# Performance work log

Measured on AMD Instinct MI355X. Metric: run time of the kernel, lower is better.

The kernel has to match this reference:

```python
import jax, jax.numpy as jnp
import numpy as np

T, N, D, H = 128, 512, 1024, 1024
LN_EPS = 1e-5


def setup_inputs() -> dict:
    key = jax.random.key(0)
    ks = jax.random.split(key, 6)
    x = jax.random.normal(ks[0], (T * N, D), jnp.float32)
    hxs = jax.random.normal(ks[1], (N, 1, H), jnp.float32)
    # binary done-masks (float, mostly 1.0 = keep hidden state, 0.0 = episode reset)
    masks = (jax.random.uniform(ks[2], (T * N, 1)) < 0.95).astype(jnp.float32)
    s = 1.0 / np.sqrt(H)
    # PyTorch GRU packed gates, order (r, z, n): weight_ih_l0 [3H, D], weight_hh_l0 [3H, H]
    W_ih = jax.random.normal(ks[3], (3 * H, D), jnp.float32) * s
    W_hh = jax.random.normal(ks[4], (3 * H, H), jnp.float32) * s
    b_ih = jnp.zeros((3 * H,), jnp.float32)  # module inits biases to 0
    b_hh = jnp.zeros((3 * H,), jnp.float32)
    gamma = jnp.ones((H,), jnp.float32)
    beta = jnp.zeros((H,), jnp.float32)
    return dict(x=x, hxs=hxs, masks=masks, W_ih=W_ih, W_hh=W_hh,
                b_ih=b_ih, b_hh=b_hh, gamma=gamma, beta=beta)


def reference(x, hxs, masks, W_ih, W_hh, b_ih, b_hh, gamma, beta):
    TN = x.shape[0]
    Nn = hxs.shape[0]
    Tt = TN // Nn
    Hd = hxs.shape[-1]
    xs = x.reshape(Tt, Nn, -1)          # [T, N, D]
    m = masks.reshape(Tt, Nn)           # [T, N]
    # Chunk starts per source: t=0 plus every t>=1 where (masks[t] == 1).any().
    # At a chunk start the hidden state is multiplied by masks[t] (broadcast over layers);
    # a scan with a per-step conditional mask-multiply is exactly equivalent to the
    # torch loop over chunks.
    reset = jnp.concatenate([jnp.ones((1,), bool), jnp.any(m[1:] == 1.0, axis=-1)])
    # Batch the input projection across all T*N tokens (one big GEMM): [T, N, 3H]
    xp = jnp.einsum('tnd,gd->tng', xs, W_ih) + b_ih
    h0 = hxs[:, 0, :]                   # recurrent_N == 1 -> [N, H]

    def step(h, inp):
        xp_t, m_t, r_t = inp
        h = jnp.where(r_t, h * m_t[:, None], h)
        hp = h @ W_hh.T + b_hh          # [N, 3H]
        xr, xz, xn = jnp.split(xp_t, 3, axis=-1)
        hr, hz, hn = jnp.split(hp, 3, axis=-1)
        r = jax.nn.sigmoid(xr + hr)
        z = jax.nn.sigmoid(xz + hz)
        n = jnp.tanh(xn + r * hn)
        h_new = (1.0 - z) * n + z * h
        return h_new, h_new

    h_last, outs = jax.lax.scan(step, h0, (xp, m, reset))
    y = outs.reshape(Tt * Nn, Hd)
    # LayerNorm over last dim
    mu = y.mean(-1, keepdims=True)
    var = y.var(-1, keepdims=True)
    y = (y - mu) * jax.lax.rsqrt(var + LN_EPS) * gamma + beta
    return y, h_last[:, None, :]
```

## Files before the change

kernel.cpp:

```cpp
#include <hip/hip_runtime.h>

#define T_STEPS 128
#define N_B     512
#define D_IN    1024
#define H_DIM   1024
#define G_DIM   3072
#define M_ALL   (T_STEPS * N_B)

typedef short          s8v  __attribute__((ext_vector_type(8)));
typedef float          f4v  __attribute__((ext_vector_type(4)));
typedef unsigned short u4v  __attribute__((ext_vector_type(4)));

__device__ __forceinline__ unsigned short f2bf(float f) {
  union { float f; unsigned u; } v; v.f = f;
  unsigned r = v.u + 0x7FFFu + ((v.u >> 16) & 1u);
  return (unsigned short)(r >> 16);
}
__device__ __forceinline__ float bf2f(unsigned short h) {
  union { unsigned u; float f; } v; v.u = ((unsigned)h) << 16;
  return v.f;
}
__device__ __forceinline__ void async16(const void* g, void* l) {
  __builtin_amdgcn_global_load_lds(
      (const __attribute__((address_space(1))) unsigned*)g,
      (__attribute__((address_space(3))) unsigned*)l, 16, 0, 0);
}
__device__ __forceinline__ float sigmoidf_(float x) { return 1.f / (1.f + __expf(-x)); }
__device__ __forceinline__ float tanhf_(float x)    { return 1.f - 2.f / (1.f + __expf(2.f * x)); }

__global__ void cvt_bf16(const float* __restrict__ in, unsigned short* __restrict__ out, long n4) {
  long i = (long)blockIdx.x * blockDim.x + threadIdx.x;
  long stride = (long)gridDim.x * blockDim.x;
  for (; i < n4; i += stride) {
    f4v v = *(const f4v*)(in + i * 4);
    u4v o;
    #pragma unroll
    for (int e = 0; e < 4; ++e) o[e] = f2bf(v[e]);
    *(u4v*)(out + i * 4) = o;
  }
}

__global__ void reset_kernel(const float* __restrict__ masks, int* __restrict__ reset) {
  const int t = blockIdx.x;
  __shared__ int flag;
  if (threadIdx.x == 0) flag = (t == 0) ? 1 : 0;
  __syncthreads();
  if (t > 0 && masks[(size_t)t * N_B + threadIdx.x] == 1.0f) flag = 1;
  __syncthreads();
  if (threadIdx.x == 0) reset[t] = flag;
}

__global__ __launch_bounds__(256) void gemm_xp(const unsigned short* __restrict__ A,
                                               const unsigned short* __restrict__ B,
                                               const float* __restrict__ bias,
                                               unsigned short* __restrict__ C) {
  const int m0 = blockIdx.y * 128, g0 = blockIdx.x * 128;
  const int tid = threadIdx.x, wv = tid >> 6, l = tid & 63;
  const int l15 = l & 15, l4 = l >> 4;
  const int wr = wv >> 1, wc = wv & 1;
  __shared__ unsigned short As[128 * 64], Bs[128 * 64];

  f4v zero4 = {0.f, 0.f, 0.f, 0.f};
  f4v acc[4][4];
  #pragma unroll
  for (int i = 0; i < 4; ++i)
    #pragma unroll
    for (int j = 0; j < 4; ++j) acc[i][j] = zero4;

  const int srow = l >> 3;
  const int selem = (l & 7) * 8;

  for (int kt = 0; kt < 1024; kt += 64) {
    #pragma unroll
    for (int cc = 0; cc < 4; ++cc) {
      int s = wv * 4 + cc;
      int row = s * 8 + srow;
      async16(A + (size_t)(m0 + row) * 1024 + kt + selem, &As[s * 512]);
      async16(B + (size_t)(g0 + row) * 1024 + kt + selem, &Bs[s * 512]);
    }
    __syncthreads();
    #pragma unroll
    for (int ks = 0; ks < 2; ++ks) {
      s8v a[4], b[4];
      #pragma unroll
      for (int i = 0; i < 4; ++i) {
        a[i] = *(const s8v*)&As[(wr * 64 + i * 16 + l15) * 64 + ks * 32 + l4 * 8];
        b[i] = *(const s8v*)&Bs[(wc * 64 + i * 16 + l15) * 64 + ks * 32 + l4 * 8];
      }
      #pragma unroll
      for (int i = 0; i < 4; ++i)
        #pragma unroll
        for (int j = 0; j < 4; ++j)
          acc[i][j] = __builtin_amdgcn_mfma_f32_16x16x32_bf16(a[i], b[j], acc[i][j], 0, 0, 0);
    }
    __syncthreads();
  }
  #pragma unroll
  for (int j = 0; j < 4; ++j) {
    int gcol = g0 + wc * 64 + j * 16 + l15;
    float bv = bias[gcol];
    #pragma unroll
    for (int i = 0; i < 4; ++i) {
      int mrow = m0 + wr * 64 + i * 16 + l4 * 4;
      #pragma unroll
      for (int r = 0; r < 4; ++r)
        C[(size_t)(mrow + r) * G_DIM + gcol] = f2bf(acc[i][j][r] + bv);
    }
  }
}

__global__ __launch_bounds__(256) void gru_step6(
    const unsigned short* __restrict__ Whh,
    const unsigned short* __restrict__ xp,
    const float* __restrict__ masks,
    const int* __restrict__ reset,
    const float* __restrict__ bhh,
    const float* __restrict__ hxs,
    const unsigned short* __restrict__ hread,
    unsigned short* __restrict__ hwrite,
    float* __restrict__ y,
    float* __restrict__ hlast,
    int t) {
  const int bid = blockIdx.x;
  const int jt = bid & 31, nt = bid >> 5;
  const int j0 = jt * 32, n0 = nt * 64;
  const int tid = threadIdx.x, w = tid >> 6, l = tid & 63;
  const int l15 = l & 15, l4 = l >> 4;
  const int wn = w & 1, wj = w >> 1;
  const size_t NH = (size_t)N_B * H_DIM;

  __shared__ unsigned short Hs[3][64 * 128];
  __shared__ unsigned short Ws[3][96 * 128];

  const int lrow4 = l >> 4;
  const int lcb = (l & 15) * 16;
  const int swz_rd = (l15 & 7) << 4;

  const int jj = j0 + wj * 16 + l15;
  const int rst = reset[t];
  const unsigned short* xpt = xp + (size_t)t * N_B * G_DIM;

  bool zo[2];
  #pragma unroll
  for (int i = 0; i < 2; ++i) {
    float mv = masks[(size_t)t * N_B + n0 + wn * 32 + i * 16 + l15];
    zo[i] = rst && (mv == 0.0f);
  }
  const float* hsrc = (t == 0) ? hxs : (y + (size_t)(t - 1) * NH);
  float hreg[2][4], mreg[2][4];
  unsigned short xpr[2][4][3];
  #pragma unroll
  for (int i = 0; i < 2; ++i)
    #pragma unroll
    for (int r = 0; r < 4; ++r) {
      const int n = n0 + wn * 32 + i * 16 + l4 * 4 + r;
      hreg[i][r] = hsrc[(size_t)n * H_DIM + jj];
      mreg[i][r] = masks[(size_t)t * N_B + n];
      const size_t xo = (size_t)n * G_DIM + jj;
      #pragma unroll
      for (int g3 = 0; g3 < 3; ++g3)
        xpr[i][r][g3] = xpt[xo + (size_t)g3 * H_DIM];
    }
  const float br = bhh[jj];
  const float bz = bhh[H_DIM + jj];
  const float bn = bhh[2 * H_DIM + jj];

  f4v zero4 = {0.f, 0.f, 0.f, 0.f};
  s8v zer8 = {0, 0, 0, 0, 0, 0, 0, 0};
  f4v acc[2][3];
  #pragma unroll
  for (int i = 0; i < 2; ++i)
    #pragma unroll
    for (int g3 = 0; g3 < 3; ++g3) acc[i][g3] = zero4;

  auto stage = [&](int buf, int kt) {
    #pragma unroll
    for (int q = 0; q < 4; ++q) {
      int rb = w * 16 + q * 4;
      int row = rb + lrow4;
      int cb = lcb ^ ((row & 7) << 4);
      async16(hread + (size_t)(n0 + row) * H_DIM + kt * 128 + (cb >> 1), &Hs[buf][rb * 128]);
    }
    #pragma unroll
    for (int q = 0; q < 6; ++q) {
      int rb = w * 24 + q * 4;
      int row = rb + lrow4;
      int gate = row >> 5, jjl = row & 31;
      int cb = lcb ^ ((row & 7) << 4);
      async16(Whh + ((size_t)gate * H_DIM + j0 + jjl) * H_DIM + kt * 128 + (cb >> 1),
              &Ws[buf][rb * 128]);
    }
  };

  stage(0, 0);
  stage(1, 1);

  #pragma unroll
  for (int kt = 0; kt < 8; ++kt) {
    if (kt < 7) asm volatile("s_waitcnt vmcnt(10)" ::: "memory");
    else        asm volatile("s_waitcnt vmcnt(0)"  ::: "memory");
    __builtin_amdgcn_s_barrier();
    __builtin_amdgcn_sched_barrier(0);
    if (kt < 6) stage((kt + 2) % 3, kt + 2);
    const char* hb = (const char*)&Hs[kt % 3][0];
    const char* wb = (const char*)&Ws[kt % 3][0];
    #pragma unroll
    for (int ks = 0; ks < 4; ++ks) {
      const int kbb = (ks * 64 + l4 * 16) ^ swz_rd;
      s8v a[2], b[3];
      #pragma unroll
      for (int i = 0; i < 2; ++i) {
        a[i] = *(const s8v*)(hb + (wn * 32 + i * 16 + l15) * 256 + kbb);
        if (zo[i]) a[i] = zer8;
      }
      #pragma unroll
      for (int g3 = 0; g3 < 3; ++g3)
        b[g3] = *(const s8v*)(wb + (g3 * 32 + wj * 16 + l15) * 256 + kbb);
      #pragma unroll
      for (int i = 0; i < 2; ++i)
        #pragma unroll
        for (int g3 = 0; g3 < 3; ++g3)
          acc[i][g3] = __builtin_amdgcn_mfma_f32_16x16x32_bf16(a[i], b[g3], acc[i][g3], 0, 0, 0);
    }
  }

  #pragma unroll
  for (int i = 0; i < 2; ++i) {
    #pragma unroll
    for (int r = 0; r < 4; ++r) {
      const int n = n0 + wn * 32 + i * 16 + l4 * 4 + r;
      float hprev = hreg[i][r];
      if (rst && mreg[i][r] == 0.0f) hprev = 0.0f;
      const float hr = acc[i][0][r] + br;
      const float hz = acc[i][1][r] + bz;
      const float hn = acc[i][2][r] + bn;
      const float xr = bf2f(xpr[i][r][0]);
      const float xz = bf2f(xpr[i][r][1]);
      const float xn = bf2f(xpr[i][r][2]);
      const float rg = sigmoidf_(xr + hr);
      const float zg = sigmoidf_(xz + hz);
      const float ng = tanhf_(xn + rg * hn);
      const float hnew = (1.f - zg) * ng + zg * hprev;
      const size_t gidx = (size_t)n * H_DIM + jj;
      y[(size_t)t * NH + gidx] = hnew;
      hwrite[gidx] = f2bf(hnew);
      if (t == T_STEPS - 1) hlast[gidx] = hnew;
    }
  }
}

__global__ __launch_bounds__(256) void ln_kernel(float* __restrict__ y,
                                                 const float* __restrict__ gamma,
                                                 const float* __restrict__ beta) {
  const size_t row = blockIdx.x;
  float* p = y + row * (size_t)H_DIM;
  const int tid = threadIdx.x;
  f4v v = *(const f4v*)(p + tid * 4);
  float s = v[0] + v[1] + v[2] + v[3];
  float q = v[0] * v[0] + v[1] * v[1] + v[2] * v[2] + v[3] * v[3];
  #pragma unroll
  for (int off = 32; off > 0; off >>= 1) {
    s += __shfl_down(s, off);
    q += __shfl_down(q, off);
  }
  __shared__ float sb[8];
  const int wid = tid >> 6, lid = tid & 63;
  if (lid == 0) { sb[wid] = s; sb[4 + wid] = q; }
  __syncthreads();
  float S = sb[0] + sb[1] + sb[2] + sb[3];
  float Q = sb[4] + sb[5] + sb[6] + sb[7];
  float mean = S * (1.f / H_DIM);
  float var = Q * (1.f / H_DIM) - mean * mean;
  float inv = rsqrtf(var + 1e-5f);
  f4v g4 = *(const f4v*)(gamma + tid * 4);
  f4v b4 = *(const f4v*)(beta + tid * 4);
  f4v o;
  #pragma unroll
  for (int e = 0; e < 4; ++e) o[e] = (v[e] - mean) * inv * g4[e] + b4[e];
  *(f4v*)(p + tid * 4) = o;
}

extern "C" void kernel_launch(void* const* d_in, const int* in_sizes, int n_in,
                              void* d_out, int out_size, void* d_ws, size_t ws_size,
                              hipStream_t stream) {
  const float* x     = (const float*)d_in[0];
  const float* hxs   = (const float*)d_in[1];
  const float* masks = (const float*)d_in[2];
  const float* W_ih  = (const float*)d_in[3];
  const float* W_hh  = (const float*)d_in[4];
  const float* b_ih  = (const float*)d_in[5];
  const float* b_hh  = (const float*)d_in[6];
  const float* gamma = (const float*)d_in[7];
  const float* beta  = (const float*)d_in[8];
  float* y = (float*)d_out;
  float* hlast = y + (size_t)T_STEPS * N_B * H_DIM;

  char* ws = (char*)d_ws;
  unsigned short* Wih_bf = (unsigned short*)ws;  ws += (size_t)G_DIM * D_IN * 2;
  unsigned short* Whh_bf = (unsigned short*)ws;  ws += (size_t)G_DIM * H_DIM * 2;
  unsigned short* xc_bf  = (unsigned short*)ws;  ws += (size_t)M_ALL * D_IN * 2;
  unsigned short* xp_bf  = (unsigned short*)ws;  ws += (size_t)M_ALL * G_DIM * 2;
  unsigned short* hbuf   = (unsigned short*)ws;  ws += (size_t)2 * N_B * H_DIM * 2;
  int* reset             = (int*)ws;             ws += 512;

  cvt_bf16<<<1024, 256, 0, stream>>>(W_ih, Wih_bf, (long)G_DIM * D_IN / 4);
  cvt_bf16<<<1024, 256, 0, stream>>>(W_hh, Whh_bf, (long)G_DIM * H_DIM / 4);
  cvt_bf16<<<512, 256, 0, stream>>>(hxs, hbuf, (long)N_B * H_DIM / 4);
  reset_kernel<<<128, 512, 0, stream>>>(masks, reset);
  cvt_bf16<<<4096, 256, 0, stream>>>(x, xc_bf, (long)M_ALL * D_IN / 4);

  dim3 gg(G_DIM / 128, M_ALL / 128);
  gemm_xp<<<gg, 256, 0, stream>>>(xc_bf, Wih_bf, b_ih, xp_bf);

  const size_t NH = (size_t)N_B * H_DIM;
  for (int t = 0; t < T_STEPS; ++t) {
    const unsigned short* hread = hbuf + (size_t)(t & 1) * NH;
    unsigned short* hwrite = hbuf + (size_t)((t & 1) ^ 1) * NH;
    gru_step6<<<256, 256, 0, stream>>>(Whh_bf, xp_bf, masks, reset, b_hh,
                                       hxs, hread, hwrite, y, hlast, t);
  }

  ln_kernel<<<T_STEPS * N_B, 256, 0, stream>>>(y, gamma, beta);
}
```

Baseline: 2.577 ms.

## Transpose xp layout, async-stage gate inputs in LDS, swizzle GEMM LDS reads

The input-projection GEMM now writes xp transposed (gate-major, token-minor) with vectorized 4-element stores and uses XOR-swizzled LDS tiles to reduce bank conflicts. Each GRU step kernel async-loads its xp slice into LDS alongside the W_hh/H pipeline instead of doing scattered per-thread 2-byte global loads. The previous hidden state is read from a compact double-buffered fp32 buffer rather than the large y tensor. The K loop is unrolled explicitly with a third prefetch stage and tuned vmcnt waits. This costs extra LDS, extra global writes for the fp32 hidden copy, and relies on the hand-tuned waitcnt values being correct.

Measured after the change: 2.483 ms. -3.6%, faster.

```diff
diff --git a/kernel.cpp b/kernel.cpp
--- a/kernel.cpp
+++ b/kernel.cpp
@@ -68,7 +68,8 @@
     for (int j = 0; j < 4; ++j) acc[i][j] = zero4;
 
   const int srow = l >> 3;
-  const int selem = (l & 7) * 8;
+  const int selem = ((l & 7) ^ srow) * 8;
+  const int swz_rd = (l15 & 7) << 4;
 
   for (int kt = 0; kt < 1024; kt += 64) {
     #pragma unroll
@@ -84,8 +85,10 @@
       s8v a[4], b[4];
       #pragma unroll
       for (int i = 0; i < 4; ++i) {
-        a[i] = *(const s8v*)&As[(wr * 64 + i * 16 + l15) * 64 + ks * 32 + l4 * 8];
-        b[i] = *(const s8v*)&Bs[(wc * 64 + i * 16 + l15) * 64 + ks * 32 + l4 * 8];
+        int ra = wr * 64 + i * 16 + l15, rb = wc * 64 + i * 16 + l15;
+        int cb = (ks * 64 + l4 * 16) ^ swz_rd;
+        a[i] = *(const s8v*)((const char*)As + ra * 128 + cb);
+        b[i] = *(const s8v*)((const char*)Bs + rb * 128 + cb);
       }
       #pragma unroll
       for (int i = 0; i < 4; ++i)
@@ -102,22 +105,25 @@
     #pragma unroll
     for (int i = 0; i < 4; ++i) {
       int mrow = m0 + wr * 64 + i * 16 + l4 * 4;
+      u4v o;
       #pragma unroll
-      for (int r = 0; r < 4; ++r)
-        C[(size_t)(mrow + r) * G_DIM + gcol] = f2bf(acc[i][j][r] + bv);
-    }
-  }
-}
-
-__global__ __launch_bounds__(256) void gru_step6(
+      for (int r = 0; r < 4; ++r) o[r] = f2bf(acc[i][j][r] + bv);
+      *(u4v*)(C + (size_t)gcol * M_ALL + mrow) = o;
+    }
+  }
+}
+
+__global__ __launch_bounds__(256) void gru_step7(
     const unsigned short* __restrict__ Whh,
-    const unsigned short* __restrict__ xp,
+    const unsigned short* __restrict__ xpT,
     const float* __restrict__ masks,
     const int* __restrict__ reset,
     const float* __restrict__ bhh,
     const float* __restrict__ hxs,
     const unsigned short* __restrict__ hread,
     unsigned short* __restrict__ hwrite,
+    const float* __restrict__ hf32r,
+    float* __restrict__ hf32w,
     float* __restrict__ y,
     float* __restrict__ hlast,
     int t) {
@@ -131,6 +137,7 @@
 
   __shared__ unsigned short Hs[3][64 * 128];
   __shared__ unsigned short Ws[3][96 * 128];
+  __shared__ unsigned short xpl[3][32][64];
 
   const int lrow4 = l >> 4;
   const int lcb = (l & 15) * 16;
@@ -138,7 +145,6 @@
 
   const int jj = j0 + wj * 16 + l15;
   const int rst = reset[t];
-  const unsigned short* xpt = xp + (size_t)t * N_B * G_DIM;
 
   bool zo[2];
   #pragma unroll
@@ -146,9 +152,8 @@
     float mv = masks[(size_t)t * N_B + n0 + wn * 32 + i * 16 + l15];
     zo[i] = rst && (mv == 0.0f);
   }
-  const float* hsrc = (t == 0) ? hxs : (y + (size_t)(t - 1) * NH);
+  const float* hsrc = (t == 0) ? hxs : hf32r;
   float hreg[2][4], mreg[2][4];
-  unsigned short xpr[2][4][3];
   #pragma unroll
   for (int i = 0; i < 2; ++i)
     #pragma unroll
@@ -156,10 +161,6 @@
       const int n = n0 + wn * 32 + i * 16 + l4 * 4 + r;
       hreg[i][r] = hsrc[(size_t)n * H_DIM + jj];
       mreg[i][r] = masks[(size_t)t * N_B + n];
-      const size_t xo = (size_t)n * G_DIM + jj;
-      #pragma unroll
-      for (int g3 = 0; g3 < 3; ++g3)
-        xpr[i][r][g3] = xpt[xo + (size_t)g3 * H_DIM];
     }
   const float br = bhh[jj];
   const float bz = bhh[H_DIM + jj];
@@ -192,51 +193,73 @@
     }
   };
 
-  stage(0, 0);
-  stage(1, 1);
-
-  #pragma unroll
-  for (int kt = 0; kt < 8; ++kt) {
-    if (kt < 7) asm volatile("s_waitcnt vmcnt(10)" ::: "memory");
-    else        asm volatile("s_waitcnt vmcnt(0)"  ::: "memory");
-    __builtin_amdgcn_s_barrier();
-    __builtin_amdgcn_sched_barrier(0);
-    if (kt < 6) stage((kt + 2) % 3, kt + 2);
-    const char* hb = (const char*)&Hs[kt % 3][0];
-    const char* wb = (const char*)&Ws[kt % 3][0];
-    #pragma unroll
-    for (int ks = 0; ks < 4; ++ks) {
-      const int kbb = (ks * 64 + l4 * 16) ^ swz_rd;
-      s8v a[2], b[3];
-      #pragma unroll
-      for (int i = 0; i < 2; ++i) {
-        a[i] = *(const s8v*)(hb + (wn * 32 + i * 16 + l15) * 256 + kbb);
-        if (zo[i]) a[i] = zer8;
-      }
-      #pragma unroll
-      for (int g3 = 0; g3 < 3; ++g3)
-        b[g3] = *(const s8v*)(wb + (g3 * 32 + wj * 16 + l15) * 256 + kbb);
-      #pragma unroll
-      for (int i = 0; i < 2; ++i)
-        #pragma unroll
-        for (int g3 = 0; g3 < 3; ++g3)
-          acc[i][g3] = __builtin_amdgcn_mfma_f32_16x16x32_bf16(a[i], b[g3], acc[i][g3], 0, 0, 0);
-    }
-  }
+  stage(0, 0); stage(1, 1); stage(2, 2);
+
+  {
+    const int jl = w * 8 + (l >> 3);
+    const int nelem = ((l & 7) ^ (l >> 3)) * 8;
+    #pragma unroll
+    for (int g3 = 0; g3 < 3; ++g3)
+      async16(xpT + (size_t)(g3 * H_DIM + j0 + jl) * M_ALL + (size_t)t * N_B + n0 + nelem,
+              &xpl[g3][w * 8][0]);
+  }
+
+#define KT_BODY(KT, VM, DO_STAGE)                                              \
+  {                                                                            \
+    asm volatile("s_waitcnt vmcnt(" #VM ")" ::: "memory");                     \
+    __builtin_amdgcn_s_barrier();                                              \
+    __builtin_amdgcn_sched_barrier(0);                                         \
+    if (DO_STAGE) stage((KT + 2) % 3, KT + 2);                                 \
+    const char* hb = (const char*)&Hs[KT % 3][0];                              \
+    const char* wb = (const char*)&Ws[KT % 3][0];                              \
+    _Pragma("unroll")                                                          \
+    for (int ks = 0; ks < 4; ++ks) {                                           \
+      const int kbb = (ks * 64 + l4 * 16) ^ swz_rd;                            \
+      s8v a[2], b[3];                                                          \
+      _Pragma("unroll")                                                        \
+      for (int i = 0; i < 2; ++i) {                                            \
+        a[i] = *(const s8v*)(hb + (wn * 32 + i * 16 + l15) * 256 + kbb);       \
+        if (zo[i]) a[i] = zer8;                                                \
+      }                                                                        \
+      _Pragma("unroll")                                                        \
+      for (int g3 = 0; g3 < 3; ++g3)                                           \
+        b[g3] = *(const s8v*)(wb + (g3 * 32 + wj * 16 + l15) * 256 + kbb);     \
+      _Pragma("unroll")                                                        \
+      for (int i = 0; i < 2; ++i)                                              \
+        _Pragma("unroll")                                                      \
+        for (int g3 = 0; g3 < 3; ++g3)                                         \
+          acc[i][g3] = __builtin_amdgcn_mfma_f32_16x16x32_bf16(a[i], b[g3],    \
+                                                              acc[i][g3], 0, 0, 0); \
+    }                                                                          \
+  }
+
+  KT_BODY(0, 23, false)
+  KT_BODY(1, 13, true)
+  KT_BODY(2, 13, true)
+  KT_BODY(3, 10, true)
+  KT_BODY(4, 10, true)
+  KT_BODY(5, 10, true)
+  KT_BODY(6, 10, false)
+  KT_BODY(7, 0,  false)
+#undef KT_BODY
 
   #pragma unroll
   for (int i = 0; i < 2; ++i) {
     #pragma unroll
     for (int r = 0; r < 4; ++r) {
       const int n = n0 + wn * 32 + i * 16 + l4 * 4 + r;
+      const int nl = wn * 32 + i * 16 + l4 * 4 + r;
+      const int jl = wj * 16 + l15;
       float hprev = hreg[i][r];
       if (rst && mreg[i][r] == 0.0f) hprev = 0.0f;
       const float hr = acc[i][0][r] + br;
       const float hz = acc[i][1][r] + bz;
       const float hn = acc[i][2][r] + bn;
-      const float xr = bf2f(xpr[i][r][0]);
-      const float xz = bf2f(xpr[i][r][1]);
-      const float xn = bf2f(xpr[i][r][2]);
+      const char* xb = (const char*)&xpl[0][0][0];
+      const int nb = (nl * 2) ^ ((jl & 7) << 4);
+      const float xr = bf2f(*(const unsigned short*)(xb + 0 * 4096 + jl * 128 + nb));
+      const float xz = bf2f(*(const unsigned short*)(xb + 1 * 4096 + jl * 128 + nb));
+      const float xn = bf2f(*(const unsigned short*)(xb + 2 * 4096 + jl * 128 + nb));
       const float rg = sigmoidf_(xr + hr);
       const float zg = sigmoidf_(xz + hz);
       const float ng = tanhf_(xn + rg * hn);
@@ -244,6 +267,7 @@
       const size_t gidx = (size_t)n * H_DIM + jj;
       y[(size_t)t * NH + gidx] = hnew;
       hwrite[gidx] = f2bf(hnew);
+      hf32w[gidx] = hnew;
       if (t == T_STEPS - 1) hlast[gidx] = hnew;
     }
   }
@@ -299,8 +323,9 @@
   unsigned short* Wih_bf = (unsigned short*)ws;  ws += (size_t)G_DIM * D_IN * 2;
   unsigned short* Whh_bf = (unsigned short*)ws;  ws += (size_t)G_DIM * H_DIM * 2;
   unsigned short* xc_bf  = (unsigned short*)ws;  ws += (size_t)M_ALL * D_IN * 2;
-  unsigned short* xp_bf  = (unsigned short*)ws;  ws += (size_t)M_ALL * G_DIM * 2;
+  unsigned short* xpT_bf = (unsigned short*)ws;  ws += (size_t)G_DIM * M_ALL * 2;
   unsigned short* hbuf   = (unsigned short*)ws;  ws += (size_t)2 * N_B * H_DIM * 2;
+  float* hf32            = (float*)ws;           ws += (size_t)2 * N_B * H_DIM * 4;
   int* reset             = (int*)ws;             ws += 512;
 
   cvt_bf16<<<1024, 256, 0, stream>>>(W_ih, Wih_bf, (long)G_DIM * D_IN / 4);
@@ -310,14 +335,16 @@
   cvt_bf16<<<4096, 256, 0, stream>>>(x, xc_bf, (long)M_ALL * D_IN / 4);
 
   dim3 gg(G_DIM / 128, M_ALL / 128);
-  gemm_xp<<<gg, 256, 0, stream>>>(xc_bf, Wih_bf, b_ih, xp_bf);
+  gemm_xp<<<gg, 256, 0, stream>>>(xc_bf, Wih_bf, b_ih, xpT_bf);
 
   const size_t NH = (size_t)N_B * H_DIM;
   for (int t = 0; t < T_STEPS; ++t) {
     const unsigned short* hread = hbuf + (size_t)(t & 1) * NH;
     unsigned short* hwrite = hbuf + (size_t)((t & 1) ^ 1) * NH;
-    gru_step6<<<256, 256, 0, stream>>>(Whh_bf, xp_bf, masks, reset, b_hh,
-                                       hxs, hread, hwrite, y, hlast, t);
+    const float* hf32r = hf32 + (size_t)(t & 1) * NH;
+    float* hf32w = hf32 + (size_t)((t & 1) ^ 1) * NH;
+    gru_step7<<<256, 256, 0, stream>>>(Whh_bf, xpT_bf, masks, reset, b_hh,
+                                       hxs, hread, hwrite, hf32r, hf32w, y, hlast, t);
   }
 
   ln_kernel<<<T_STEPS * N_B, 256, 0, stream>>>(y, gamma, beta);
```
